# Performance work log

Measured on AMD Instinct MI355X. Metric: run time of the kernel, lower is better.

The kernel has to match this reference:

```python
import jax, jax.numpy as jnp
import numpy as np

B, N, DIM = 8, 2048, 1024
HEADS, CB_DIM, CB_SIZE = 8, 64, 1024
CB_IN = HEADS * CB_DIM  # 512


def setup_inputs() -> dict:
    key = jax.random.key(0)
    ks = jax.random.split(key, 4)
    x = jax.random.normal(ks[0], (B, N, DIM), dtype=jnp.float32)
    W_in = jax.random.normal(ks[1], (DIM, CB_IN), dtype=jnp.float32) * (DIM ** -0.5)
    b_in = jnp.zeros((CB_IN,), dtype=jnp.float32)
    W_out = jax.random.normal(ks[2], (CB_IN, DIM), dtype=jnp.float32) * (CB_IN ** -0.5)
    b_out = jnp.zeros((DIM,), dtype=jnp.float32)
    embed = jax.random.normal(ks[3], (CB_SIZE, CB_DIM), dtype=jnp.float32)
    return {"x": x, "W_in": W_in, "b_in": b_in, "W_out": W_out, "b_out": b_out, "embed": embed}


def reference(x, W_in, b_in, W_out, b_out, embed):
    # project_in: [B, N, DIM] -> [B, N, HEADS*CB_DIM]
    h = jnp.einsum("bnd,de->bne", x, W_in) + b_in
    # multi-head split, shared codebook: 'b n (h d) -> (b h) n d' view as [B, N, H, d]
    hx = h.reshape(B, N, HEADS, CB_DIM)
    # euclidean nearest neighbor: argmin ||hx - e||^2 == argmax (2 hx.e - ||e||^2)
    dots = jnp.einsum("bnhd,cd->bnhc", hx, embed)          # [B, N, H, C]
    e_sq = jnp.sum(embed * embed, axis=-1)                    # [C]
    scores = 2.0 * dots - e_sq                                 # monotone in -dist
    embed_ind = jnp.argmax(scores, axis=-1)                    # [B, N, H] int
    quantize = embed[embed_ind]                                # [B, N, H, d] gather
    # merge heads and project_out
    q = quantize.reshape(B, N, CB_IN)
    out = jnp.einsum("bne,ed->bnd", q, W_out) + b_out          # [B, N, DIM]
    return out, embed_ind
```

## Files before the change

kernel.cpp:

```cpp
#include <hip/hip_runtime.h>

#define B_      8
#define N_      2048
#define DIM_    1024
#define HEADS_  8
#define CBD_    64
#define CBS_    1024
#define CBIN_   512
#define M_      (B_*N_)
#define M2_     (M_*HEADS_)

#define MARGIN 0.02f
#define XSTR   40

typedef unsigned short ushort_t;
typedef __attribute__((ext_vector_type(8))) short short8;
typedef __attribute__((ext_vector_type(4))) float f32x4;

__device__ inline ushort_t f2bf(float f) {
    unsigned int u = __builtin_bit_cast(unsigned int, f);
    unsigned int r = u + 0x7FFFu + ((u >> 16) & 1u);
    return (ushort_t)(r >> 16);
}
__device__ inline float bf2f(ushort_t h) {
    unsigned int u = ((unsigned int)h) << 16;
    return __builtin_bit_cast(float, u);
}
__device__ inline f32x4 mfma_bf16(short8 a, short8 b, f32x4 c) {
    return __builtin_amdgcn_mfma_f32_16x16x32_bf16(a, b, c, 0, 0, 0);
}
__device__ inline void store4u(ushort_t* p, ushort_t a, ushort_t b, ushort_t c, ushort_t d) {
    uint2 u;
    u.x = (unsigned int)a | ((unsigned int)b << 16);
    u.y = (unsigned int)c | ((unsigned int)d << 16);
    *(uint2*)p = u;
}
__device__ inline void split3(float f, ushort_t& s1, ushort_t& s2, ushort_t& s3) {
    s1 = f2bf(f);
    float r = f - bf2f(s1);
    s2 = f2bf(r);
    float r2 = r - bf2f(s2);
    s3 = f2bf(r2);
}
__device__ inline void async_cp16(void* lds, const void* g) {
    __builtin_amdgcn_global_load_lds(
        (const __attribute__((address_space(1))) unsigned int*)g,
        (__attribute__((address_space(3))) unsigned int*)lds, 16, 0, 0);
}

__global__ __launch_bounds__(256) void prep_embed(const float* __restrict__ embed,
                                                  ushort_t* __restrict__ hi,
                                                  ushort_t* __restrict__ lo,
                                                  float* __restrict__ esq) {
    int i = blockIdx.x * 256 + threadIdx.x;
    int code = i >> 6, d = i & 63;
    float f = embed[i];
    int dst = code * 64 + ((((d >> 3) ^ (code & 7)) << 3) | (d & 7));
    ushort_t hh = f2bf(f);
    hi[dst] = hh;
    lo[dst] = f2bf(f - bf2f(hh));
    float s = f * f;
#pragma unroll
    for (int m = 1; m <= 32; m <<= 1) s += __shfl_xor(s, m);
    if (d == 0) esq[code] = s;
}

__global__ __launch_bounds__(256) void transposeW(const float* __restrict__ W,
                                                  ushort_t* __restrict__ WT) {
    __shared__ ushort_t t[64][65];
    const int tid = threadIdx.x;
    const int n0 = blockIdx.x * 64, k0 = blockIdx.y * 64;
#pragma unroll
    for (int s = 0; s < 16; ++s) {
        int i = s * 256 + tid;
        int r = i >> 6, c = i & 63;
        t[r][c] = f2bf(W[(size_t)(k0 + r) * DIM_ + n0 + c]);
    }
    __syncthreads();
#pragma unroll
    for (int s = 0; s < 16; ++s) {
        int i = s * 256 + tid;
        int r = i >> 6, c = i & 63;
        WT[(size_t)(n0 + r) * CBIN_ + k0 + c] = t[c][r];
    }
}

__global__ __launch_bounds__(256) void split_WinT(const float* __restrict__ W,
                                                  ushort_t* __restrict__ W1T,
                                                  ushort_t* __restrict__ W2T,
                                                  ushort_t* __restrict__ W3T) {
    __shared__ ushort_t t1[64][65];
    __shared__ ushort_t t2[64][65];
    __shared__ ushort_t t3[64][65];
    const int tid = threadIdx.x;
    const int n0 = blockIdx.x * 64, k0 = blockIdx.y * 64;
#pragma unroll
    for (int s = 0; s < 16; ++s) {
        int i = s * 256 + tid;
        int r = i >> 6, c = i & 63;
        float f = W[(size_t)(k0 + r) * CBIN_ + n0 + c];
        split3(f, t1[r][c], t2[r][c], t3[r][c]);
    }
    __syncthreads();
#pragma unroll
    for (int s = 0; s < 16; ++s) {
        int i = s * 256 + tid;
        int r = i >> 6, c = i & 63;
        size_t o = (size_t)(n0 + r) * DIM_ + k0 + c;
        W1T[o] = t1[c][r];
        W2T[o] = t2[c][r];
        W3T[o] = t3[c][r];
    }
}

__global__ __launch_bounds__(512) void gemm_in_x6(const float* __restrict__ x,
                                                  const ushort_t* __restrict__ W1T,
                                                  const ushort_t* __restrict__ W2T,
                                                  const ushort_t* __restrict__ W3T,
                                                  const float* __restrict__ bias,
                                                  float* __restrict__ C) {
    __shared__ ushort_t A1[128 * XSTR];
    __shared__ ushort_t A2[128 * XSTR];
    __shared__ ushort_t A3[128 * XSTR];
    __shared__ ushort_t B1[128 * XSTR];
    __shared__ ushort_t B2[128 * XSTR];
    __shared__ ushort_t B3[128 * XSTR];

    const int tid  = threadIdx.x;
    const int lane = tid & 63;
    const int w    = tid >> 6;
    const int quad = lane >> 4;
    const int col  = lane & 15;

    const int slot   = blockIdx.y * 4 + blockIdx.x;
    const int g      = slot & 7;
    const int t      = slot >> 3;
    const int m0     = (g + 8 * (t >> 2)) * 128;
    const int n0     = (t & 3) * 128;

    const int wm   = (w & 1) * 64;
    const int wn   = (w >> 1) * 32;

    f32x4 acc[4][2];
#pragma unroll
    for (int rt = 0; rt < 4; ++rt)
#pragma unroll
        for (int ct = 0; ct < 2; ++ct) acc[rt][ct] = (f32x4){0.f, 0.f, 0.f, 0.f};

    for (int k0 = 0; k0 < DIM_; k0 += 32) {
        __syncthreads();
#pragma unroll
        for (int s = 0; s < 2; ++s) {
            int f = s * 512 + tid;
            int row = f >> 3, qq = f & 7;
            float4 v = *(const float4*)(x + (size_t)(m0 + row) * DIM_ + k0 + qq * 4);
            float vv[4] = {v.x, v.y, v.z, v.w};
            ushort_t p1[4], p2[4], p3[4];
#pragma unroll
            for (int j = 0; j < 4; ++j) split3(vv[j], p1[j], p2[j], p3[j]);
            int base = row * XSTR + qq * 4;
            store4u(&A1[base], p1[0], p1[1], p1[2], p1[3]);
            store4u(&A2[base], p2[0], p2[1], p2[2], p2[3]);
            store4u(&A3[base], p3[0], p3[1], p3[2], p3[3]);
        }
        {
            int row = tid >> 2, g2 = tid & 3;
            size_t go = (size_t)(n0 + row) * DIM_ + k0 + g2 * 8;
            int lo = row * XSTR + g2 * 8;
            *(uint4*)&B1[lo] = *(const uint4*)(W1T + go);
            *(uint4*)&B2[lo] = *(const uint4*)(W2T + go);
            *(uint4*)&B3[lo] = *(const uint4*)(W3T + go);
        }
        __syncthreads();

        short8 a1[4], a2[4], a3[4], b1[2], b2[2], b3[2];
#pragma unroll
        for (int rt = 0; rt < 4; ++rt) {
            int o = (wm + rt * 16 + col) * XSTR + quad * 8;
            a1[rt] = *(const short8*)&A1[o];
            a2[rt] = *(const short8*)&A2[o];
            a3[rt] = *(const short8*)&A3[o];
        }
#pragma unroll
        for (int ct = 0; ct < 2; ++ct) {
            int o = (wn + ct * 16 + col) * XSTR + quad * 8;
            b1[ct] = *(const short8*)&B1[o];
            b2[ct] = *(const short8*)&B2[o];
            b3[ct] = *(const short8*)&B3[o];
        }
#define COMBO(AP, BP)                                                   \
        _Pragma("unroll")                                               \
        for (int ct = 0; ct < 2; ++ct)                                  \
            _Pragma("unroll")                                           \
            for (int rt = 0; rt < 4; ++rt)                              \
                acc[rt][ct] = mfma_bf16(AP[rt], BP[ct], acc[rt][ct]);
        COMBO(a1, b1); COMBO(a1, b2); COMBO(a2, b1);
        COMBO(a2, b2); COMBO(a1, b3); COMBO(a3, b1);
#undef COMBO
    }

#pragma unroll
    for (int ct = 0; ct < 2; ++ct) {
        int gc = n0 + wn + ct * 16 + col;
        float bb = bias[gc];
#pragma unroll
        for (int rt = 0; rt < 4; ++rt) {
#pragma unroll
            for (int reg = 0; reg < 4; ++reg) {
                int gr = m0 + wm + rt * 16 + quad * 4 + reg;
                C[(size_t)gr * CBIN_ + gc] = acc[rt][ct][reg] + bb;
            }
        }
    }
}

__global__ __launch_bounds__(512, 4) void argmax2(const float* __restrict__ h,
                                                  const ushort_t* __restrict__ ehswz,
                                                  const ushort_t* __restrict__ elswz,
                                                  const float* __restrict__ esq,
                                                  const float* __restrict__ embed,
                                                  float* __restrict__ outIdxF,
                                                  int* __restrict__ outIdxI) {
    __shared__ ushort_t EB[2][2][4096];
    __shared__ float    ESQ[CBS_];
    __shared__ int BIDX[256];
    __shared__ int FLAG[256];
    __shared__ int NFLAG;

    const int tid  = threadIdx.x;
    const int lane = tid & 63;
    const int w    = tid >> 6;
    const int quad = lane >> 4;
    const int col  = lane & 15;
    const int r0   = blockIdx.x * 256;

    if (tid == 0) NFLAG = 0;
    if (tid < 256) *(float4*)&ESQ[tid * 4] = *(const float4*)(esq + tid * 4);

    short8 AH[2][2], AL[2][2];
#pragma unroll
    for (int rt = 0; rt < 2; ++rt) {
        const float* hp = h + (size_t)(r0 + w * 32 + rt * 16 + col) * 64 + quad * 8;
#pragma unroll
        for (int ks = 0; ks < 2; ++ks) {
            float4 u0 = *(const float4*)(hp + ks * 32);
            float4 u1 = *(const float4*)(hp + ks * 32 + 4);
            float vv[8] = {u0.x, u0.y, u0.z, u0.w, u1.x, u1.y, u1.z, u1.w};
            short8 hh, ll;
#pragma unroll
            for (int j = 0; j < 8; ++j) {
                ushort_t hi = f2bf(vv[j]);
                hh[j] = (short)hi;
                ll[j] = (short)f2bf(vv[j] - bf2f(hi));
            }
            AH[rt][ks] = hh;
            AL[rt][ks] = ll;
        }
    }

#define STAGE(ch, b)                                                          \
    do {                                                                      \
        int eo = (ch) * 4096 + tid * 8;                                       \
        int wo = w * 512;                                                     \
        async_cp16(&EB[b][0][wo], ehswz + eo);                                \
        async_cp16(&EB[b][1][wo], elswz + eo);                                \
    } while (0)

    STAGE(0, 0);

    float v1[8], v2[8];
    int   i1[8];
#pragma unroll
    for (int s = 0; s < 8; ++s) { v1[s] = -3.4e38f; v2[s] = -3.4e38f; i1[s] = 0; }

    __syncthreads();

    int cur = 0;
    for (int ch = 0; ch < 16; ++ch) {
        if (ch < 15) STAGE(ch + 1, cur ^ 1);
#pragma unroll
        for (int ct = 0; ct < 4; ++ct) {
            const int lc = ct * 16 + col;
            const int x7 = col & 7;
            const int o0 = lc * 64 + (((quad)     ^ x7) << 3);
            const int o1 = lc * 64 + (((quad + 4) ^ x7) << 3);
            short8 BH0 = *(const short8*)&EB[cur][0][o0];
            short8 BH1 = *(const short8*)&EB[cur][0][o1];
            short8 BL0 = *(const short8*)&EB[cur][1][o0];
            short8 BL1 = *(const short8*)&EB[cur][1][o1];
            const int code = ch * 64 + lc;
            float eq = ESQ[code];
#pragma unroll
            for (int rt = 0; rt < 2; ++rt) {
                f32x4 acc = {0.f, 0.f, 0.f, 0.f};
                acc = mfma_bf16(AH[rt][0], BH0, acc);
                acc = mfma_bf16(AH[rt][1], BH1, acc);
                acc = mfma_bf16(AH[rt][0], BL0, acc);
                acc = mfma_bf16(AH[rt][1], BL1, acc);
                acc = mfma_bf16(AL[rt][0], BH0, acc);
                acc = mfma_bf16(AL[rt][1], BH1, acc);
#pragma unroll
                for (int reg = 0; reg < 4; ++reg) {
                    const int st = rt * 4 + reg;
                    float sc = fmaf(2.f, acc[reg], -eq);
                    v2[st] = __builtin_amdgcn_fmed3f(sc, v1[st], v2[st]);
                    bool gt = sc > v1[st];
                    v1[st] = fmaxf(v1[st], sc);
                    i1[st] = gt ? code : i1[st];
                }
            }
        }
        __syncthreads();
        cur ^= 1;
    }
#undef STAGE

#pragma unroll
    for (int st = 0; st < 8; ++st) {
#pragma unroll
        for (int m = 1; m <= 8; m <<= 1) {
            float ov1 = __shfl_xor(v1[st], m);
            int   oi1 = __shfl_xor(i1[st], m);
            float ov2 = __shfl_xor(v2[st], m);
            float losr = fminf(v1[st], ov1);
            v2[st] = fmaxf(fmaxf(v2[st], ov2), losr);
            bool take = (ov1 > v1[st]) || (ov1 == v1[st] && oi1 < i1[st]);
            v1[st] = take ? ov1 : v1[st];
            i1[st] = take ? oi1 : i1[st];
        }
        if (col == 0) {
            int rt = st >> 2, reg = st & 3;
            int row_l = w * 32 + rt * 16 + quad * 4 + reg;
            BIDX[row_l] = i1[st];
            if (v1[st] - v2[st] < MARGIN) {
                int p = atomicAdd(&NFLAG, 1);
                FLAG[p] = row_l;
            }
        }
    }
    __syncthreads();

    int nf = NFLAG;
    for (int i = w; i < nf; i += 8) {
        int row_l = FLAG[i];
        const float* hr = h + (size_t)(r0 + row_l) * 64;
        float accf[16];
#pragma unroll
        for (int j = 0; j < 16; ++j) accf[j] = 0.f;
        for (int d4 = 0; d4 < 16; ++d4) {
            float4 hv = *(const float4*)(hr + d4 * 4);
#pragma unroll
            for (int j = 0; j < 16; ++j) {
                int c = lane + 64 * j;
                float4 ev = *(const float4*)(embed + (size_t)c * 64 + d4 * 4);
                accf[j] += hv.x * ev.x + hv.y * ev.y + hv.z * ev.z + hv.w * ev.w;
            }
        }
        float best = -3.4e38f; int bi = 0;
#pragma unroll
        for (int j = 0; j < 16; ++j) {
            int c = lane + 64 * j;
            float sc = 2.f * accf[j] - ESQ[c];
            if (sc > best) { best = sc; bi = c; }
        }
#pragma unroll
        for (int m = 1; m <= 32; m <<= 1) {
            float ob = __shfl_xor(best, m);
            int  obi = __shfl_xor(bi, m);
            if (ob > best || (ob == best && obi < bi)) { best = ob; bi = obi; }
        }
        if (lane == 0) BIDX[row_l] = bi;
    }
    __syncthreads();

    if (tid < 256) {
        int b = BIDX[tid];
        outIdxF[r0 + tid] = (float)b;
        outIdxI[r0 + tid] = b;
    }
}

__global__ __launch_bounds__(256) void gemm_out_bf16(const ushort_t* __restrict__ ehswz,
                                                     const int* __restrict__ idx,
                                                     const ushort_t* __restrict__ WbfT,
                                                     const float* __restrict__ bias,
                                                     float* __restrict__ C) {
    __shared__ ushort_t Qs[2][8192];
    __shared__ ushort_t Ws[2][8192];
    __shared__ int idxs[128 * HEADS_];

    const int tid  = threadIdx.x;
    const int lane = tid & 63;
    const int w    = tid >> 6;
    const int quad = lane >> 4;
    const int col  = lane & 15;
    const int m0   = blockIdx.y * 128;
    const int n0   = blockIdx.x * 128;
    const int wm   = (w & 1) * 64;
    const int wn   = (w >> 1) * 64;

#pragma unroll
    for (int s = 0; s < 4; ++s) {
        int f = s * 256 + tid;
        idxs[f] = idx[(size_t)m0 * HEADS_ + f];
    }
    __syncthreads();

#define STAGEO(hd, b)                                                         \
    do {                                                                      \
        _Pragma("unroll")                                                     \
        for (int j2 = 0; j2 < 2; ++j2) {                                      \
            const int j = w * 2 + j2;                                         \
            _Pragma("unroll")                                                 \
            for (int r2 = 0; r2 < 2; ++r2) {                                  \
                const int row = r2 * 64 + lane;                               \
                const int e   = idxs[row * HEADS_ + (hd)];                    \
                async_cp16(&Qs[b][(j * 128 + r2 * 64) * 8],                   \
                           ehswz + (size_t)e * 64 + ((j ^ (e & 7)) << 3));    \
                async_cp16(&Ws[b][(j * 128 + r2 * 64) * 8],                   \
                           WbfT + (size_t)(n0 + row) * CBIN_ + (hd)*64 + j*8);\
            }                                                                 \
        }                                                                     \
    } while (0)

    f32x4 acc[4][4];
#pragma unroll
    for (int rt = 0; rt < 4; ++rt)
#pragma unroll
        for (int ct = 0; ct < 4; ++ct) acc[rt][ct] = (f32x4){0.f, 0.f, 0.f, 0.f};

    STAGEO(0, 0);
    __syncthreads();

    int b = 0;
#pragma unroll 1
    for (int hd = 0; hd < HEADS_; ++hd) {
        if (hd < 7) STAGEO(hd + 1, b ^ 1);
#pragma unroll
        for (int ks = 0; ks < 2; ++ks) {
            const int sbase = ((ks * 4 + quad) * 128) * 8;
            short8 a[4], bb[4];
#pragma unroll
            for (int rt = 0; rt < 4; ++rt)
                a[rt] = *(const short8*)&Qs[b][sbase + (wm + rt * 16 + col) * 8];
#pragma unroll
            for (int ct = 0; ct < 4; ++ct)
                bb[ct] = *(const short8*)&Ws[b][sbase + (wn + ct * 16 + col) * 8];
#pragma unroll
            for (int rt = 0; rt < 4; ++rt)
#pragma unroll
                for (int ct = 0; ct < 4; ++ct)
                    acc[rt][ct] = mfma_bf16(a[rt], bb[ct], acc[rt][ct]);
        }
        __syncthreads();
        b ^= 1;
    }
#undef STAGEO

#pragma unroll
    for (int ct = 0; ct < 4; ++ct) {
        int gc = n0 + wn + ct * 16 + col;
        float bbias = bias[gc];
#pragma unroll
        for (int rt = 0; rt < 4; ++rt) {
#pragma unroll
            for (int reg = 0; reg < 4; ++reg) {
                int gr = m0 + wm + rt * 16 + quad * 4 + reg;
                C[(size_t)gr * DIM_ + gc] = acc[rt][ct][reg] + bbias;
            }
        }
    }
}

extern "C" void kernel_launch(void* const* d_in, const int* in_sizes, int n_in,
                              void* d_out, int out_size, void* d_ws, size_t ws_size,
                              hipStream_t stream) {
    const float* x     = (const float*)d_in[0];
    const float* W_in  = (const float*)d_in[1];
    const float* b_in  = (const float*)d_in[2];
    const float* W_out = (const float*)d_in[3];
    const float* b_out = (const float*)d_in[4];
    const float* embed = (const float*)d_in[5];

    float* out     = (float*)d_out;
    float* outIdxF = out + (size_t)M_ * DIM_;

    char* ws = (char*)d_ws;
    float*    h     = (float*)ws;
    int*      idxI  = (int*)(ws + 33554432);
    float*    esq   = (float*)(ws + 34078720);
    ushort_t* ehswz = (ushort_t*)(ws + 34082816);
    ushort_t* elswz = (ushort_t*)(ws + 34213888);
    ushort_t* WbfT  = (ushort_t*)(ws + 34344960);
    ushort_t* W1T   = (ushort_t*)(ws + 35393536);
    ushort_t* W2T   = (ushort_t*)(ws + 36442112);
    ushort_t* W3T   = (ushort_t*)(ws + 37490688);

    prep_embed<<<dim3(CBS_ * CBD_ / 256), dim3(256), 0, stream>>>(embed, ehswz, elswz, esq);
    transposeW<<<dim3(DIM_ / 64, CBIN_ / 64), dim3(256), 0, stream>>>(W_out, WbfT);
    split_WinT<<<dim3(CBIN_ / 64, DIM_ / 64), dim3(256), 0, stream>>>(W_in, W1T, W2T, W3T);
    gemm_in_x6<<<dim3(CBIN_ / 128, M_ / 128), dim3(512), 0, stream>>>(x, W1T, W2T, W3T,
                                                                      b_in, h);
    argmax2<<<dim3(M2_ / 256), dim3(512), 0, stream>>>(h, ehswz, elswz, esq, embed,
                                                       outIdxF, idxI);
    gemm_out_bf16<<<dim3(DIM_ / 128, M_ / 128), dim3(256), 0, stream>>>(ehswz, idxI, WbfT,
                                                                        b_out, out);
}
```

Before: 346.5 us.

## Shrink argmax tile to 64 rows per 256-thread block with smaller codebook chunks

Retiles the argmax kernel from 256 rows per 512-thread block to 64 rows per 256-thread block. Each wave now handles one 16-row tile instead of two, and the codebook is streamed in 32-code chunks over 32 iterations instead of 64-code chunks over 16. The shared ESQ copy is dropped in favour of direct global loads of esq. The aim is to cut LDS use and register pressure and launch more blocks for better occupancy, at the cost of less codebook reuse per staged chunk and more barriers per row.

```diff
diff --git a/kernel.cpp b/kernel.cpp
--- a/kernel.cpp
+++ b/kernel.cpp
@@ -214,17 +214,16 @@
     }
 }
 
-__global__ __launch_bounds__(512, 4) void argmax2(const float* __restrict__ h,
+__global__ __launch_bounds__(256, 4) void argmax2(const float* __restrict__ h,
                                                   const ushort_t* __restrict__ ehswz,
                                                   const ushort_t* __restrict__ elswz,
                                                   const float* __restrict__ esq,
                                                   const float* __restrict__ embed,
                                                   float* __restrict__ outIdxF,
                                                   int* __restrict__ outIdxI) {
-    __shared__ ushort_t EB[2][2][4096];
-    __shared__ float    ESQ[CBS_];
-    __shared__ int BIDX[256];
-    __shared__ int FLAG[256];
+    __shared__ ushort_t EB[2][2][2048];
+    __shared__ int BIDX[64];
+    __shared__ int FLAG[64];
     __shared__ int NFLAG;
 
     const int tid  = threadIdx.x;
@@ -232,15 +231,13 @@
     const int w    = tid >> 6;
     const int quad = lane >> 4;
     const int col  = lane & 15;
-    const int r0   = blockIdx.x * 256;
+    const int r0   = blockIdx.x * 64;
 
     if (tid == 0) NFLAG = 0;
-    if (tid < 256) *(float4*)&ESQ[tid * 4] = *(const float4*)(esq + tid * 4);
-
-    short8 AH[2][2], AL[2][2];
-#pragma unroll
-    for (int rt = 0; rt < 2; ++rt) {
-        const float* hp = h + (size_t)(r0 + w * 32 + rt * 16 + col) * 64 + quad * 8;
+
+    short8 AH[2], AL[2];
+    {
+        const float* hp = h + (size_t)(r0 + w * 16 + col) * 64 + quad * 8;
 #pragma unroll
         for (int ks = 0; ks < 2; ++ks) {
             float4 u0 = *(const float4*)(hp + ks * 32);
@@ -253,14 +250,14 @@
                 hh[j] = (short)hi;
                 ll[j] = (short)f2bf(vv[j] - bf2f(hi));
             }
-            AH[rt][ks] = hh;
-            AL[rt][ks] = ll;
+            AH[ks] = hh;
+            AL[ks] = ll;
         }
     }
 
 #define STAGE(ch, b)                                                          \
     do {                                                                      \
-        int eo = (ch) * 4096 + tid * 8;                                       \
+        int eo = (ch) * 2048 + tid * 8;                                       \
         int wo = w * 512;                                                     \
         async_cp16(&EB[b][0][wo], ehswz + eo);                                \
         async_cp16(&EB[b][1][wo], elswz + eo);                                \
@@ -268,18 +265,20 @@
 
     STAGE(0, 0);
 
-    float v1[8], v2[8];
-    int   i1[8];
-#pragma unroll
-    for (int s = 0; s < 8; ++s) { v1[s] = -3.4e38f; v2[s] = -3.4e38f; i1[s] = 0; }
+    float v1[4], v2[4];
+    int   i1[4];
+#pragma unroll
+    for (int s = 0; s < 4; ++s) { v1[s] = -3.4e38f; v2[s] = -3.4e38f; i1[s] = 0; }
 
     __syncthreads();
 
     int cur = 0;
-    for (int ch = 0; ch < 16; ++ch) {
-        if (ch < 15) STAGE(ch + 1, cur ^ 1);
-#pragma unroll
-        for (int ct = 0; ct < 4; ++ct) {
+    for (int ch = 0; ch < 32; ++ch) {
+        if (ch < 31) STAGE(ch + 1, cur ^ 1);
+        float eq0 = esq[ch * 32 + col];
+        float eq1 = esq[ch * 32 + 16 + col];
+#pragma unroll
+        for (int ct = 0; ct < 2; ++ct) {
             const int lc = ct * 16 + col;
             const int x7 = col & 7;
             const int o0 = lc * 64 + (((quad)     ^ x7) << 3);
@@ -288,26 +287,22 @@
             short8 BH1 = *(const short8*)&EB[cur][0][o1];
             short8 BL0 = *(const short8*)&EB[cur][1][o0];
             short8 BL1 = *(const short8*)&EB[cur][1][o1];
-            const int code = ch * 64 + lc;
-            float eq = ESQ[code];
-#pragma unroll
-            for (int rt = 0; rt < 2; ++rt) {
-                f32x4 acc = {0.f, 0.f, 0.f, 0.f};
-                acc = mfma_bf16(AH[rt][0], BH0, acc);
-                acc = mfma_bf16(AH[rt][1], BH1, acc);
-                acc = mfma_bf16(AH[rt][0], BL0, acc);
-                acc = mfma_bf16(AH[rt][1], BL1, acc);
-                acc = mfma_bf16(AL[rt][0], BH0, acc);
-                acc = mfma_bf16(AL[rt][1], BH1, acc);
-#pragma unroll
-                for (int reg = 0; reg < 4; ++reg) {
-                    const int st = rt * 4 + reg;
-                    float sc = fmaf(2.f, acc[reg], -eq);
-                    v2[st] = __builtin_amdgcn_fmed3f(sc, v1[st], v2[st]);
-                    bool gt = sc > v1[st];
-                    v1[st] = fmaxf(v1[st], sc);
-                    i1[st] = gt ? code : i1[st];
-                }
+            const int code = ch * 32 + lc;
+            const float eq = ct ? eq1 : eq0;
+            f32x4 acc = {0.f, 0.f, 0.f, 0.f};
+            acc = mfma_bf16(AH[0], BH0, acc);
+            acc = mfma_bf16(AH[1], BH1, acc);
+            acc = mfma_bf16(AH[0], BL0, acc);
+            acc = mfma_bf16(AH[1], BL1, acc);
+            acc = mfma_bf16(AL[0], BH0, acc);
+            acc = mfma_bf16(AL[1], BH1, acc);
+#pragma unroll
+            for (int reg = 0; reg < 4; ++reg) {
+                float sc = fmaf(2.f, acc[reg], -eq);
+                v2[reg] = __builtin_amdgcn_fmed3f(sc, v1[reg], v2[reg]);
+                bool gt = sc > v1[reg];
+                v1[reg] = fmaxf(v1[reg], sc);
+                i1[reg] = gt ? code : i1[reg];
             }
         }
         __syncthreads();
@@ -316,7 +311,7 @@
 #undef STAGE
 
 #pragma unroll
-    for (int st = 0; st < 8; ++st) {
+    for (int st = 0; st < 4; ++st) {
 #pragma unroll
         for (int m = 1; m <= 8; m <<= 1) {
             float ov1 = __shfl_xor(v1[st], m);
@@ -329,8 +324,7 @@
             i1[st] = take ? oi1 : i1[st];
         }
         if (col == 0) {
-            int rt = st >> 2, reg = st & 3;
-            int row_l = w * 32 + rt * 16 + quad * 4 + reg;
+            int row_l = w * 16 + quad * 4 + st;
             BIDX[row_l] = i1[st];
             if (v1[st] - v2[st] < MARGIN) {
                 int p = atomicAdd(&NFLAG, 1);
@@ -341,7 +335,7 @@
     __syncthreads();
 
     int nf = NFLAG;
-    for (int i = w; i < nf; i += 8) {
+    for (int i = w; i < nf; i += 4) {
         int row_l = FLAG[i];
         const float* hr = h + (size_t)(r0 + row_l) * 64;
         float accf[16];
@@ -360,7 +354,7 @@
 #pragma unroll
         for (int j = 0; j < 16; ++j) {
             int c = lane + 64 * j;
-            float sc = 2.f * accf[j] - ESQ[c];
+            float sc = 2.f * accf[j] - esq[c];
             if (sc > best) { best = sc; bi = c; }
         }
 #pragma unroll
@@ -373,7 +367,7 @@
     }
     __syncthreads();
 
-    if (tid < 256) {
+    if (tid < 64) {
         int b = BIDX[tid];
         outIdxF[r0 + tid] = (float)b;
         outIdxI[r0 + tid] = b;
@@ -501,8 +495,8 @@
     split_WinT<<<dim3(CBIN_ / 64, DIM_ / 64), dim3(256), 0, stream>>>(W_in, W1T, W2T, W3T);
     gemm_in_x6<<<dim3(CBIN_ / 128, M_ / 128), dim3(512), 0, stream>>>(x, W1T, W2T, W3T,
                                                                       b_in, h);
-    argmax2<<<dim3(M2_ / 256), dim3(512), 0, stream>>>(h, ehswz, elswz, esq, embed,
-                                                       outIdxF, idxI);
+    argmax2<<<dim3(M2_ / 64), dim3(256), 0, stream>>>(h, ehswz, elswz, esq, embed,
+                                                      outIdxF, idxI);
     gemm_out_bf16<<<dim3(DIM_ / 128, M_ / 128), dim3(256), 0, stream>>>(ehswz, idxI, WbfT,
                                                                         b_out, out);
 }
```

After: 350.8 us. Within noise of the previous version (+1.3%).
